# Kernel optimization log

Hardware: AMD Instinct MI355X
Metric: run time of the kernel (lower is better)

The kernel has to match this reference:

```python
import jax, jax.numpy as jnp
import numpy as np

NB_FRAMES = 16384


def setup_inputs() -> dict:
    key = jax.random.key(0)
    x = jax.random.randint(key, (4096, 1), 0, NB_FRAMES, dtype=jnp.int64 if jax.config.jax_enable_x64 else jnp.int32)
    # The module's buffer: identity matrix cast to the working dtype.
    eye = jnp.eye(NB_FRAMES, dtype=jnp.float32)
    return {"eye": eye, "x": x}


def reference(eye, x):
    # Faithful vectorized form of: cat([eye[x_flat[i]] for i ...]).view(bs, *inter, nb_frames)
    bs = x.shape[0]
    inter = x.shape[1:-1]  # dims between batch and the trailing index dim
    x_flat = x.reshape(-1)
    out = eye[x_flat]                       # [bs*prod(inter), nb_frames] gather of one-hot rows
    return out.reshape(bs, *inter, NB_FRAMES)
```

## Files before the change

kernel.cpp:

```cpp
#include <hip/hip_runtime.h>
#include <hip/hip_bf16.h>


#define NB_FRAMES 16384

__global__ void onehot_scatter_kernel(const int* __restrict__ x,
                                      float* __restrict__ out,
                                      int n) {
    int i = blockIdx.x * blockDim.x + threadIdx.x;
    if (i < n) {
        int col = x[i];
        if (col >= 0 && col < NB_FRAMES) {
            out[(size_t)i * NB_FRAMES + col] = 1.0f;
        }
    }
}

extern "C" void kernel_launch(void* const* d_in, const int* in_sizes, int n_in,
                              void* d_out, int out_size, void* d_ws, size_t ws_size,
                              hipStream_t stream) {
    const int* x = (const int*)d_in[1];
    float* out = (float*)d_out;
    int n = in_sizes[1];

    hipMemsetAsync(out, 0, (size_t)out_size * sizeof(float), stream);

    int block = 256;
    int grid = (n + block - 1) / block;
    onehot_scatter_kernel<<<grid, block, 0, stream>>>(x, out, n);
}
```

Before: 1.211 ms.

## Fuse zero-fill and one-hot scatter into single row-wise vectorized write kernel

Replaces the separate memset plus scatter kernel with one kernel where each block writes an entire output row using float4 stores, inserting the 1.0 in the matching lane. This removes the second pass over the output and the extra launch, and makes the writes fully coalesced. It assumes the output size is a multiple of the row length and drops the bounds check on the index.

```diff
diff --git a/kernel.cpp b/kernel.cpp
--- a/kernel.cpp
+++ b/kernel.cpp
@@ -3,16 +3,27 @@
 
 
 #define NB_FRAMES 16384
+#define F4_PER_ROW (NB_FRAMES / 4)
+#define BLOCK 256
+#define F4_PER_THREAD (F4_PER_ROW / BLOCK)
 
-__global__ void onehot_scatter_kernel(const int* __restrict__ x,
-                                      float* __restrict__ out,
-                                      int n) {
-    int i = blockIdx.x * blockDim.x + threadIdx.x;
-    if (i < n) {
-        int col = x[i];
-        if (col >= 0 && col < NB_FRAMES) {
-            out[(size_t)i * NB_FRAMES + col] = 1.0f;
+__global__ __launch_bounds__(BLOCK) void onehot_rows_kernel(
+        const int* __restrict__ x, float4* __restrict__ out) {
+    const int row = blockIdx.x;
+    const int col = x[row];
+
+    float4* rowp = out + (size_t)row * F4_PER_ROW;
+    const float4 z = make_float4(0.f, 0.f, 0.f, 0.f);
+
+    #pragma unroll
+    for (int j = 0; j < F4_PER_THREAD; ++j) {
+        const int f4 = j * BLOCK + threadIdx.x;
+        float4 v = z;
+        const int base = f4 * 4;
+        if (col >= base && col < base + 4) {
+            ((float*)&v)[col - base] = 1.0f;
         }
+        rowp[f4] = v;
     }
 }
 
@@ -20,12 +31,8 @@
                               void* d_out, int out_size, void* d_ws, size_t ws_size,
                               hipStream_t stream) {
     const int* x = (const int*)d_in[1];
-    float* out = (float*)d_out;
-    int n = in_sizes[1];
+    float4* out = (float4*)d_out;
+    const int n_rows = out_size / NB_FRAMES;
 
-    hipMemsetAsync(out, 0, (size_t)out_size * sizeof(float), stream);
-
-    int block = 256;
-    int grid = (n + block - 1) / block;
-    onehot_scatter_kernel<<<grid, block, 0, stream>>>(x, out, n);
+    onehot_rows_kernel<<<n_rows, BLOCK, 0, stream>>>(x, out);
 }
```

New measurement: 1.228 ms. No clear change (+1.4%).
